# Optimization experiments

Measured on AMD Instinct MI355X. Metric: run time of the kernel, lower is better.

The kernel has to match this reference:

```python
import jax, jax.numpy as jnp
import numpy as np

H = 100  # hidden size

def _lstm_layer(x, Wih, Whh, b):
    # x: [B, T, D_in]; Wih: [4H, D_in]; Whh: [4H, H]; b: [4H]
    # Precompute input contribution for all timesteps (batched GEMM).
    xw = jnp.einsum('btd,gd->btg', x, Wih) + b            # [B, T, 4H]
    B = x.shape[0]
    h0 = jnp.zeros((B, H), x.dtype)
    c0 = jnp.zeros((B, H), x.dtype)
    WhhT = Whh.T                                          # [H, 4H]

    def step(carry, xw_t):
        h, c = carry
        gates = xw_t + h @ WhhT                           # [B, 4H]
        i, f, g, o = jnp.split(gates, 4, axis=-1)         # PyTorch order i,f,g,o
        i = jax.nn.sigmoid(i)
        f = jax.nn.sigmoid(f)
        g = jnp.tanh(g)
        o = jax.nn.sigmoid(o)
        c = f * c + i * g
        h = o * jnp.tanh(c)
        return (h, c), h

    _, hs = jax.lax.scan(step, (h0, c0), jnp.swapaxes(xw, 0, 1))  # [T, B, H]
    return jnp.swapaxes(hs, 0, 1)                         # [B, T, H]


def setup_inputs() -> dict:
    key = jax.random.key(0)
    ks = jax.random.split(key, 12)
    B, T = 512, 512
    s = 0.08  # small init scale to avoid gate saturation
    return {
        'z':    jax.random.normal(ks[0], (B, T, 1), jnp.float32),
        'Wih0': jax.random.normal(ks[1], (4 * H, 1), jnp.float32) * s,
        'Whh0': jax.random.normal(ks[2], (4 * H, H), jnp.float32) * s,
        'b0':   jax.random.normal(ks[3], (4 * H,), jnp.float32) * s,
        'Wih1': jax.random.normal(ks[4], (4 * H, H), jnp.float32) * s,
        'Whh1': jax.random.normal(ks[5], (4 * H, H), jnp.float32) * s,
        'b1':   jax.random.normal(ks[6], (4 * H,), jnp.float32) * s,
        'Wih2': jax.random.normal(ks[7], (4 * H, H), jnp.float32) * s,
        'Whh2': jax.random.normal(ks[8], (4 * H, H), jnp.float32) * s,
        'b2':   jax.random.normal(ks[9], (4 * H,), jnp.float32) * s,
        'Wp':   jax.random.normal(ks[10], (1, H), jnp.float32) * s,
        'bp':   jax.random.normal(ks[11], (1,), jnp.float32) * s,
    }


def reference(z, Wih0, Whh0, b0, Wih1, Whh1, b1, Wih2, Whh2, b2, Wp, bp):
    h = _lstm_layer(z, Wih0, Whh0, b0)
    h = _lstm_layer(h, Wih1, Whh1, b1)
    h = _lstm_layer(h, Wih2, Whh2, b2)       # [B, T, H]
    return jnp.tanh(jnp.einsum('bth,oh->bto', h, Wp) + bp)  # [B, T, 1]
```

## Files before the change

kernel.cpp:

```cpp
#include <hip/hip_runtime.h>
#include <cstdint>
#include <cstddef>


#define HH 100
#define G4 400
#define NB 512
#define NT 512
#define NBG 32
#define NTILE 25
#define KP 128

typedef _Float16 f16;
typedef _Float16 f16x8 __attribute__((ext_vector_type(8)));
typedef float f32x4 __attribute__((ext_vector_type(4)));

__device__ __forceinline__ float sigm(float x) { return 1.0f / (1.0f + __expf(-x)); }
__device__ __forceinline__ float tanh_(float x) { return 1.0f - 2.0f / (__expf(2.0f * x) + 1.0f); }

#define PIN22 __attribute__((amdgpu_flat_work_group_size(512, 512), \
                             amdgpu_waves_per_eu(2, 2)))

__device__ __forceinline__ int hswz(int b2, int u) {
  return b2 * KP + ((((u >> 3) ^ (b2 & 7)) << 3) | (u & 7));
}
__device__ __forceinline__ int bswz(int b2, int j) {
  return b2 * KP + ((j ^ (b2 & 7)) << 3);
}

__global__ __launch_bounds__(256) void wprep(
    const float* __restrict__ Whh0, const float* __restrict__ Whh1,
    const float* __restrict__ Whh2, const float* __restrict__ Wih1,
    const float* __restrict__ Wih2, const float* __restrict__ b1,
    const float* __restrict__ b2, const float* __restrict__ Wih0,
    const float* __restrict__ b0,
    f16* __restrict__ wfA, f16* __restrict__ wfI,
    float* __restrict__ biasf, float* __restrict__ l0w, float* __restrict__ l0b)
{
  int idx = blockIdx.x * 256 + threadIdx.x;
  if (idx < 153600) {
    int l = idx / 51200, r = idx % 51200;
    int nt = r / 2048, r2 = r % 2048;
    int kt = r2 / 512, r3 = r2 % 512;
    int lane = r3 / 8, j = r3 % 8;
    int mp = nt * 16 + (lane & 15);
    int grow = (mp & 3) * HH + (mp >> 2);
    int k = kt * 32 + (lane >> 4) * 8 + j;
    const float* W = (l == 0) ? Whh0 : ((l == 1) ? Whh1 : Whh2);
    wfA[idx] = (k < HH) ? (f16)W[grow * HH + k] : (f16)0.0f;
    return;
  }
  idx -= 153600;
  if (idx < 102400) {
    int l = idx / 51200, r = idx % 51200;
    int nt = r / 2048, r2 = r % 2048;
    int kt = r2 / 512, r3 = r2 % 512;
    int lane = r3 / 8, j = r3 % 8;
    int mp = nt * 16 + (lane & 15);
    int grow = (mp & 3) * HH + (mp >> 2);
    int k = kt * 32 + (lane >> 4) * 8 + j;
    const float* W = (l == 0) ? Wih1 : Wih2;
    wfI[idx] = (k < HH) ? (f16)W[grow * HH + k] : (f16)0.0f;
    return;
  }
  idx -= 102400;
  if (idx < 12800) {
    int l = idx / 6400, r = idx % 6400;
    int nt = r / 256, r2 = r % 256;
    int lane = r2 / 4, rr = r2 % 4;
    int mp = nt * 16 + (lane >> 4) * 4 + rr;
    int grow = (mp & 3) * HH + (mp >> 2);
    biasf[idx] = ((l == 0) ? b1 : b2)[grow];
    return;
  }
  idx -= 12800;
  if (idx < 12800) {
    int w = idx / 6400, r = idx % 6400;
    int nt = r / 256, r2 = r % 256;
    int lane = r2 / 4, rr = r2 % 4;
    int mp = nt * 16 + (lane >> 4) * 4 + rr;
    int grow = (mp & 3) * HH + (mp >> 2);
    if (w == 0) l0w[r] = Wih0[grow];
    else        l0b[r] = b0[grow];
  }
}

__global__ PIN22 void xwp(
    const float* __restrict__ hbufT,
    const f16* __restrict__ wfIl,
    const float* __restrict__ biasl,
    float* __restrict__ xwf,
    int t0, int CT)
{
  const int tid = threadIdx.x;
  const int w = tid >> 6, lane = tid & 63;
  const int nblk = CT / 8;
  const int bg = blockIdx.x / nblk, ts = blockIdx.x % nblk;
  const int tb = t0 + ts * 8;
  const int br = lane & 15, lg = lane >> 4;

  __shared__ __align__(16) f16 x16[8][16 * KP];

  {
    uint32_t* p = (uint32_t*)&x16[0][0];
    for (int i = tid; i < 8 * 16 * KP / 2; i += 512) p[i] = 0u;
  }
  __syncthreads();
  for (int i = tid; i < 8 * HH * 16; i += 512) {
    int t = i / 1600, r = i % 1600;
    int u = r >> 4, b2 = r & 15;
    float v = hbufT[(((size_t)bg * NT + (tb + t)) * HH + u) * 16 + b2];
    x16[t][hswz(b2, u)] = (f16)v;
  }

  const int NS = (w == 7) ? 4 : 3;
  const int tbase = 3 * w;

  f16x8 A[4][4];
  f32x4 bias4[4];
#pragma unroll
  for (int s = 0; s < 4; ++s) {
    if (s < NS) {
      int nt = tbase + s;
#pragma unroll
      for (int kt = 0; kt < 4; ++kt)
        A[s][kt] = *(const f16x8*)(wfIl + ((nt * 4 + kt) * 64 + lane) * 8);
      bias4[s] = *(const f32x4*)(biasl + (nt * 64 + lane) * 4);
    }
  }
  __syncthreads();

  for (int t = 0; t < 8; ++t) {
    f16x8 B[4];
#pragma unroll
    for (int kt = 0; kt < 4; ++kt)
      B[kt] = *(const f16x8*)(&x16[t][bswz(br, (kt << 2) + lg)]);
    const int tc = ts * 8 + t;
#pragma unroll
    for (int s = 0; s < 4; ++s) {
      if (s < NS) {
        f32x4 acc = bias4[s];
#pragma unroll
        for (int kt = 0; kt < 4; ++kt)
          acc = __builtin_amdgcn_mfma_f32_16x16x32_f16(A[s][kt], B[kt], acc, 0, 0, 0);
        int nt = tbase + s;
        *(f32x4*)(xwf + ((((size_t)bg * CT + tc) * NTILE + nt) * 64 + lane) * 4) = acc;
      }
    }
  }
}

__global__ PIN22 void recx(
    const float* __restrict__ xwf,
    const f16* __restrict__ wfAl,
    float* __restrict__ hbufT,
    float* __restrict__ cbuf,
    int t0, int CT)
{
  const int tid = threadIdx.x;
  const int w = tid >> 6, lane = tid & 63;
  const int bg = blockIdx.x;
  const int br = lane & 15, lg = lane >> 4;
  const int NS = (w == 0) ? 4 : 3;

  __shared__ __align__(16) f16 hHi[2][16 * KP];
  __shared__ __align__(16) f16 hLo[2][16 * KP];

  {
    uint32_t* p0 = (uint32_t*)&hHi[0][0];
    uint32_t* p1 = (uint32_t*)&hLo[0][0];
    for (int i = tid; i < 2 * 16 * KP / 2; i += 512) { p0[i] = 0u; p1[i] = 0u; }
  }
  __syncthreads();
  if (t0 > 0) {
    for (int i = tid; i < HH * 16; i += 512) {
      int u = i >> 4, b2 = i & 15;
      float v = hbufT[(((size_t)bg * NT + (t0 - 1)) * HH + u) * 16 + b2];
      f16 hi = (f16)v;
      hHi[0][hswz(b2, u)] = hi;
      hLo[0][hswz(b2, u)] = (f16)(v - (float)hi);
    }
  }

  f16x8 A[4][4];
  float c[4] = {0.f, 0.f, 0.f, 0.f};
  f32x4 xwC[4], xwN[4];
#pragma unroll
  for (int s = 0; s < 4; ++s) {
    if (s < NS) {
      const int nt = w + 8 * s;
#pragma unroll
      for (int kt = 0; kt < 4; ++kt)
        A[s][kt] = *(const f16x8*)(wfAl + ((nt * 4 + kt) * 64 + lane) * 8);
      if (t0 > 0) c[s] = cbuf[((size_t)bg * NTILE + nt) * 64 + lane];
      xwC[s] = *(const f32x4*)(xwf + (((size_t)bg * CT * NTILE + nt) * 64 + lane) * 4);
    }
  }
  __syncthreads();

  int cur = 0;
  for (int t = 0; t < CT; ++t) {
    f16x8 Bhi[4], Blo[4];
#pragma unroll
    for (int kt = 0; kt < 4; ++kt) {
      const int pos = bswz(br, (kt << 2) + lg);
      Bhi[kt] = *(const f16x8*)(&hHi[cur][pos]);
      Blo[kt] = *(const f16x8*)(&hLo[cur][pos]);
    }
    const int tn = (t + 1 < CT) ? t + 1 : t;
#pragma unroll
    for (int s = 0; s < 4; ++s) {
      if (s < NS) {
        const int nt = w + 8 * s;
        xwN[s] = *(const f32x4*)(xwf + ((((size_t)bg * CT + tn) * NTILE + nt) * 64 + lane) * 4);
      }
    }
#pragma unroll
    for (int s = 0; s < 4; ++s) {
      if (s < NS) {
        const int nt = w + 8 * s;
        f32x4 ah = xwC[s];
        f32x4 al = {0.f, 0.f, 0.f, 0.f};
#pragma unroll
        for (int kt = 0; kt < 4; ++kt) {
          ah = __builtin_amdgcn_mfma_f32_16x16x32_f16(A[s][kt], Bhi[kt], ah, 0, 0, 0);
          al = __builtin_amdgcn_mfma_f32_16x16x32_f16(A[s][kt], Blo[kt], al, 0, 0, 0);
        }
        f32x4 acc = ah + al;
        float iv = sigm(acc.x);
        float fv = sigm(acc.y);
        float gv = tanh_(acc.z);
        float ov = sigm(acc.w);
        c[s] = fv * c[s] + iv * gv;
        float hv = ov * tanh_(c[s]);
        const int u = nt * 4 + lg;
        hbufT[(((size_t)bg * NT + (t0 + t)) * HH + u) * 16 + br] = hv;
        f16 hi = (f16)hv;
        hHi[cur ^ 1][hswz(br, u)] = hi;
        hLo[cur ^ 1][hswz(br, u)] = (f16)(hv - (float)hi);
      }
    }
    __syncthreads();
#pragma unroll
    for (int s = 0; s < 4; ++s) xwC[s] = xwN[s];
    cur ^= 1;
  }
#pragma unroll
  for (int s = 0; s < 4; ++s) {
    if (s < NS) {
      const int nt = w + 8 * s;
      cbuf[((size_t)bg * NTILE + nt) * 64 + lane] = c[s];
    }
  }
}

__global__ PIN22 void rec0(
    const float* __restrict__ z,
    const float* __restrict__ l0w,
    const float* __restrict__ l0b,
    const f16* __restrict__ wfA0,
    float* __restrict__ hbufT)
{
  const int tid = threadIdx.x;
  const int w = tid >> 6, lane = tid & 63;
  const int bg = blockIdx.x;
  const int br = lane & 15, lg = lane >> 4;
  const int NS = (w == 0) ? 4 : 3;

  __shared__ __align__(16) f16 hHi[2][16 * KP];
  __shared__ __align__(16) f16 hLo[2][16 * KP];
  __shared__ __align__(16) float zl[NT][16];

  {
    uint32_t* p0 = (uint32_t*)&hHi[0][0];
    uint32_t* p1 = (uint32_t*)&hLo[0][0];
    for (int i = tid; i < 2 * 16 * KP / 2; i += 512) { p0[i] = 0u; p1[i] = 0u; }
  }
  for (int i = tid; i < 16 * NT; i += 512) {
    int j = i / NT, t = i % NT;
    zl[t][j] = z[(size_t)(bg * 16 + j) * NT + t];
  }

  f16x8 A[4][4];
  float c[4] = {0.f, 0.f, 0.f, 0.f};
  f32x4 wv[4], bv[4];
#pragma unroll
  for (int s = 0; s < 4; ++s) {
    if (s < NS) {
      const int nt = w + 8 * s;
#pragma unroll
      for (int kt = 0; kt < 4; ++kt)
        A[s][kt] = *(const f16x8*)(wfA0 + ((nt * 4 + kt) * 64 + lane) * 8);
      wv[s] = *(const f32x4*)(l0w + (nt * 64 + lane) * 4);
      bv[s] = *(const f32x4*)(l0b + (nt * 64 + lane) * 4);
    }
  }
  __syncthreads();

  int cur = 0;
  for (int t = 0; t < NT; ++t) {
    f16x8 Bhi[4], Blo[4];
#pragma unroll
    for (int kt = 0; kt < 4; ++kt) {
      const int pos = bswz(br, (kt << 2) + lg);
      Bhi[kt] = *(const f16x8*)(&hHi[cur][pos]);
      Blo[kt] = *(const f16x8*)(&hLo[cur][pos]);
    }
    const float zv = zl[t][br];
#pragma unroll
    for (int s = 0; s < 4; ++s) {
      if (s < NS) {
        const int nt = w + 8 * s;
        f32x4 ah = bv[s] + wv[s] * zv;
        f32x4 al = {0.f, 0.f, 0.f, 0.f};
#pragma unroll
        for (int kt = 0; kt < 4; ++kt) {
          ah = __builtin_amdgcn_mfma_f32_16x16x32_f16(A[s][kt], Bhi[kt], ah, 0, 0, 0);
          al = __builtin_amdgcn_mfma_f32_16x16x32_f16(A[s][kt], Blo[kt], al, 0, 0, 0);
        }
        f32x4 acc = ah + al;
        float iv = sigm(acc.x);
        float fv = sigm(acc.y);
        float gv = tanh_(acc.z);
        float ov = sigm(acc.w);
        c[s] = fv * c[s] + iv * gv;
        float hv = ov * tanh_(c[s]);
        const int u = nt * 4 + lg;
        hbufT[(((size_t)bg * NT + t) * HH + u) * 16 + br] = hv;
        f16 hi = (f16)hv;
        hHi[cur ^ 1][hswz(br, u)] = hi;
        hLo[cur ^ 1][hswz(br, u)] = (f16)(hv - (float)hi);
      }
    }
    __syncthreads();
    cur ^= 1;
  }
}

__global__ __launch_bounds__(256) void proj(
    const float* __restrict__ hbufT,
    const float* __restrict__ Wp, const float* __restrict__ bp,
    float* __restrict__ out)
{
  const int tid = threadIdx.x;
  const int bg = blockIdx.x >> 5, tsub = blockIdx.x & 31;
  const int br = tid & 15, tl = tid >> 4;
  const int t = tsub * 16 + tl;
  const float* hp = hbufT + (((size_t)bg * NT + t) * HH) * 16 + br;
  float acc = 0.0f;
#pragma unroll 4
  for (int u = 0; u < HH; ++u) acc += hp[u * 16] * Wp[u];
  out[(size_t)(bg * 16 + br) * NT + t] = tanh_(acc + bp[0]);
}

extern "C" void kernel_launch(void* const* d_in, const int* in_sizes, int n_in,
                              void* d_out, int out_size, void* d_ws, size_t ws_size,
                              hipStream_t stream) {
  const float* z    = (const float*)d_in[0];
  const float* Wih0 = (const float*)d_in[1];
  const float* Whh0 = (const float*)d_in[2];
  const float* b0   = (const float*)d_in[3];
  const float* Wih1 = (const float*)d_in[4];
  const float* Whh1 = (const float*)d_in[5];
  const float* b1   = (const float*)d_in[6];
  const float* Wih2 = (const float*)d_in[7];
  const float* Whh2 = (const float*)d_in[8];
  const float* b2   = (const float*)d_in[9];
  const float* Wp   = (const float*)d_in[10];
  const float* bp   = (const float*)d_in[11];
  float* out = (float*)d_out;

  float* ws = (float*)d_ws;
  float* hbufT = ws;
  float* cbuf  = ws + 26214400;
  f16*   wfA   = (f16*)(ws + 26265600);
  f16*   wfI   = (f16*)(ws + 26342400);
  float* biasf = ws + 26393600;
  float* l0w   = ws + 26406400;
  float* l0b   = ws + 26412800;
  float* xwf   = ws + 26419200;

  const size_t fixed = 26419200;
  int CT = 16;
  for (int c : {128, 64, 32, 16}) {
    if ((fixed + (size_t)NBG * c * 6400) * 4 <= ws_size) { CT = c; break; }
  }

  wprep<<<1100, 256, 0, stream>>>(Whh0, Whh1, Whh2, Wih1, Wih2, b1, b2,
                                  Wih0, b0, wfA, wfI, biasf, l0w, l0b);

  rec0<<<NBG, 512, 0, stream>>>(z, l0w, l0b, wfA, hbufT);

  for (int l = 0; l < 2; ++l) {
    const f16* wfAl = wfA + (size_t)(l + 1) * 51200;
    const f16* wfIl = wfI + (size_t)l * 51200;
    const float* bfl = biasf + (size_t)l * 6400;
    for (int t0 = 0; t0 < NT; t0 += CT) {
      xwp<<<NBG * (CT / 8), 512, 0, stream>>>(hbufT, wfIl, bfl, xwf, t0, CT);
      recx<<<NBG, 512, 0, stream>>>(xwf, wfAl, hbufT, cbuf, t0, CT);
    }
  }

  proj<<<1024, 256, 0, stream>>>(hbufT, Wp, bp, out);
}
```

Baseline: 3.042 ms.

## Fuse three LSTM layers into one persistent wavefront-pipelined kernel with ring buffers

The three LSTM layers now run inside a single persistent kernel of 96 blocks, one per layer and batch group. Each block hands its per-timestep hidden states to the next layer through a small f16 ring buffer in global memory, with producer and consumer counters updated by acquire/release atomics. This lets the layers run concurrently as a wavefront instead of serially. It also removes the many xwp/recx launches and the xw round-trip through memory, because the input projection is computed inline with MFMA. The costs are spin-wait synchronization between blocks, the requirement that all 96 blocks are co-resident (otherwise it deadlocks), and f16 rounding of the inter-layer inputs.

```diff
diff --git a/kernel.cpp b/kernel.cpp
--- a/kernel.cpp
+++ b/kernel.cpp
@@ -10,6 +10,8 @@
 #define NBG 32
 #define NTILE 25
 #define KP 128
+#define XROW 104
+#define RW 16
 
 typedef _Float16 f16;
 typedef _Float16 f16x8 __attribute__((ext_vector_type(8)));
@@ -21,11 +23,28 @@
 #define PIN22 __attribute__((amdgpu_flat_work_group_size(512, 512), \
                              amdgpu_waves_per_eu(2, 2)))
 
+__device__ __forceinline__ void spin_ge(const uint32_t* p, uint32_t v) {
+  while (__hip_atomic_load(p, __ATOMIC_ACQUIRE, __HIP_MEMORY_SCOPE_AGENT) < v)
+    __builtin_amdgcn_s_sleep(2);
+}
+__device__ __forceinline__ void rel_store(uint32_t* p, uint32_t v) {
+  __hip_atomic_store(p, v, __ATOMIC_RELEASE, __HIP_MEMORY_SCOPE_AGENT);
+}
+
 __device__ __forceinline__ int hswz(int b2, int u) {
   return b2 * KP + ((((u >> 3) ^ (b2 & 7)) << 3) | (u & 7));
 }
 __device__ __forceinline__ int bswz(int b2, int j) {
   return b2 * KP + ((j ^ (b2 & 7)) << 3);
+}
+
+__global__ __launch_bounds__(256) void initk(uint32_t* __restrict__ ring_u32,
+                                             uint32_t* __restrict__ cnts) {
+  const int n_ring = 2 * NBG * RW * 16 * XROW / 2;
+  for (int i = blockIdx.x * 256 + threadIdx.x; i < n_ring; i += gridDim.x * 256)
+    ring_u32[i] = 0u;
+  int i = blockIdx.x * 256 + threadIdx.x;
+  if (i < 2048) cnts[i] = 0u;
 }
 
 __global__ __launch_bounds__(256) void wprep(
@@ -46,8 +65,8 @@
     int mp = nt * 16 + (lane & 15);
     int grow = (mp & 3) * HH + (mp >> 2);
     int k = kt * 32 + (lane >> 4) * 8 + j;
-    const float* W = (l == 0) ? Whh0 : ((l == 1) ? Whh1 : Whh2);
-    wfA[idx] = (k < HH) ? (f16)W[grow * HH + k] : (f16)0.0f;
+    const float* Wm = (l == 0) ? Whh0 : ((l == 1) ? Whh1 : Whh2);
+    wfA[idx] = (k < HH) ? (f16)Wm[grow * HH + k] : (f16)0.0f;
     return;
   }
   idx -= 153600;
@@ -59,8 +78,8 @@
     int mp = nt * 16 + (lane & 15);
     int grow = (mp & 3) * HH + (mp >> 2);
     int k = kt * 32 + (lane >> 4) * 8 + j;
-    const float* W = (l == 0) ? Wih1 : Wih2;
-    wfI[idx] = (k < HH) ? (f16)W[grow * HH + k] : (f16)0.0f;
+    const float* Wm = (l == 0) ? Wih1 : Wih2;
+    wfI[idx] = (k < HH) ? (f16)Wm[grow * HH + k] : (f16)0.0f;
     return;
   }
   idx -= 102400;
@@ -85,106 +104,45 @@
   }
 }
 
-__global__ PIN22 void xwp(
-    const float* __restrict__ hbufT,
-    const f16* __restrict__ wfIl,
-    const float* __restrict__ biasl,
-    float* __restrict__ xwf,
-    int t0, int CT)
+__global__ PIN22 void lstm3(
+    const float* __restrict__ z,
+    const float* __restrict__ l0w,
+    const float* __restrict__ l0b,
+    const f16* __restrict__ wfA,
+    const f16* __restrict__ wfI,
+    const float* __restrict__ biasf,
+    f16* __restrict__ ring,
+    float* __restrict__ hbufT,
+    uint32_t* __restrict__ prodc,
+    uint32_t* __restrict__ consc)
 {
   const int tid = threadIdx.x;
   const int w = tid >> 6, lane = tid & 63;
-  const int nblk = CT / 8;
-  const int bg = blockIdx.x / nblk, ts = blockIdx.x % nblk;
-  const int tb = t0 + ts * 8;
-  const int br = lane & 15, lg = lane >> 4;
-
-  __shared__ __align__(16) f16 x16[8][16 * KP];
-
-  {
-    uint32_t* p = (uint32_t*)&x16[0][0];
-    for (int i = tid; i < 8 * 16 * KP / 2; i += 512) p[i] = 0u;
-  }
-  __syncthreads();
-  for (int i = tid; i < 8 * HH * 16; i += 512) {
-    int t = i / 1600, r = i % 1600;
-    int u = r >> 4, b2 = r & 15;
-    float v = hbufT[(((size_t)bg * NT + (tb + t)) * HH + u) * 16 + b2];
-    x16[t][hswz(b2, u)] = (f16)v;
-  }
-
-  const int NS = (w == 7) ? 4 : 3;
-  const int tbase = 3 * w;
-
-  f16x8 A[4][4];
-  f32x4 bias4[4];
-#pragma unroll
-  for (int s = 0; s < 4; ++s) {
-    if (s < NS) {
-      int nt = tbase + s;
-#pragma unroll
-      for (int kt = 0; kt < 4; ++kt)
-        A[s][kt] = *(const f16x8*)(wfIl + ((nt * 4 + kt) * 64 + lane) * 8);
-      bias4[s] = *(const f32x4*)(biasl + (nt * 64 + lane) * 4);
-    }
-  }
-  __syncthreads();
-
-  for (int t = 0; t < 8; ++t) {
-    f16x8 B[4];
-#pragma unroll
-    for (int kt = 0; kt < 4; ++kt)
-      B[kt] = *(const f16x8*)(&x16[t][bswz(br, (kt << 2) + lg)]);
-    const int tc = ts * 8 + t;
-#pragma unroll
-    for (int s = 0; s < 4; ++s) {
-      if (s < NS) {
-        f32x4 acc = bias4[s];
-#pragma unroll
-        for (int kt = 0; kt < 4; ++kt)
-          acc = __builtin_amdgcn_mfma_f32_16x16x32_f16(A[s][kt], B[kt], acc, 0, 0, 0);
-        int nt = tbase + s;
-        *(f32x4*)(xwf + ((((size_t)bg * CT + tc) * NTILE + nt) * 64 + lane) * 4) = acc;
-      }
-    }
-  }
-}
-
-__global__ PIN22 void recx(
-    const float* __restrict__ xwf,
-    const f16* __restrict__ wfAl,
-    float* __restrict__ hbufT,
-    float* __restrict__ cbuf,
-    int t0, int CT)
-{
-  const int tid = threadIdx.x;
-  const int w = tid >> 6, lane = tid & 63;
-  const int bg = blockIdx.x;
+  const int layer = blockIdx.x >> 5;
+  const int bg = blockIdx.x & 31;
   const int br = lane & 15, lg = lane >> 4;
   const int NS = (w == 0) ? 4 : 3;
 
   __shared__ __align__(16) f16 hHi[2][16 * KP];
   __shared__ __align__(16) f16 hLo[2][16 * KP];
+  __shared__ __align__(16) float zl[NT][16];
 
   {
     uint32_t* p0 = (uint32_t*)&hHi[0][0];
     uint32_t* p1 = (uint32_t*)&hLo[0][0];
     for (int i = tid; i < 2 * 16 * KP / 2; i += 512) { p0[i] = 0u; p1[i] = 0u; }
   }
-  __syncthreads();
-  if (t0 > 0) {
-    for (int i = tid; i < HH * 16; i += 512) {
-      int u = i >> 4, b2 = i & 15;
-      float v = hbufT[(((size_t)bg * NT + (t0 - 1)) * HH + u) * 16 + b2];
-      f16 hi = (f16)v;
-      hHi[0][hswz(b2, u)] = hi;
-      hLo[0][hswz(b2, u)] = (f16)(v - (float)hi);
-    }
-  }
-
-  f16x8 A[4][4];
+  if (layer == 0) {
+    for (int i = tid; i < 16 * NT; i += 512) {
+      int j = i / NT, t = i % NT;
+      zl[t][j] = z[(size_t)(bg * 16 + j) * NT + t];
+    }
+  }
+
+  const f16* wfAl = wfA + (size_t)layer * 51200;
+  f16x8 A[4][4], AI[4][4];
+  f32x4 wv[4], bv[4], bias4[4];
   float c[4] = {0.f, 0.f, 0.f, 0.f};
-  f32x4 xwC[4], xwN[4];
 #pragma unroll
   for (int s = 0; s < 4; ++s) {
     if (s < NS) {
@@ -192,14 +150,37 @@
 #pragma unroll
       for (int kt = 0; kt < 4; ++kt)
         A[s][kt] = *(const f16x8*)(wfAl + ((nt * 4 + kt) * 64 + lane) * 8);
-      if (t0 > 0) c[s] = cbuf[((size_t)bg * NTILE + nt) * 64 + lane];
-      xwC[s] = *(const f32x4*)(xwf + (((size_t)bg * CT * NTILE + nt) * 64 + lane) * 4);
-    }
+      if (layer == 0) {
+        wv[s] = *(const f32x4*)(l0w + (nt * 64 + lane) * 4);
+        bv[s] = *(const f32x4*)(l0b + (nt * 64 + lane) * 4);
+      } else {
+        const f16* wfIl = wfI + (size_t)(layer - 1) * 51200;
+#pragma unroll
+        for (int kt = 0; kt < 4; ++kt)
+          AI[s][kt] = *(const f16x8*)(wfIl + ((nt * 4 + kt) * 64 + lane) * 8);
+        bias4[s] = *(const f32x4*)(biasf + (size_t)(layer - 1) * 6400 + (nt * 64 + lane) * 4);
+      }
+    }
+  }
+
+  uint32_t* myProd = prodc + ((size_t)layer * NBG + bg) * 16;
+  uint32_t* myCons = consc + ((size_t)layer * NBG + bg) * 16;
+  const uint32_t* upProd = prodc + ((size_t)(layer - 1) * NBG + bg) * 16;
+  uint32_t* upCons = consc + ((size_t)(layer - 1) * NBG + bg) * 16;
+  f16* myPipe = ring + ((size_t)layer * NBG + bg) * RW * 16 * XROW;
+  const f16* srcPipe = ring + ((size_t)(layer - 1) * NBG + bg) * RW * 16 * XROW;
+
+  f16x8 Bx[4];
+  if (layer >= 1) {
+    spin_ge(upProd, 1u);
+#pragma unroll
+    for (int kt = 0; kt < 4; ++kt)
+      Bx[kt] = *(const f16x8*)(srcPipe + br * XROW + kt * 32 + lg * 8);
   }
   __syncthreads();
 
   int cur = 0;
-  for (int t = 0; t < CT; ++t) {
+  for (int t = 0; t < NT; ++t) {
     f16x8 Bhi[4], Blo[4];
 #pragma unroll
     for (int kt = 0; kt < 4; ++kt) {
@@ -207,19 +188,33 @@
       Bhi[kt] = *(const f16x8*)(&hHi[cur][pos]);
       Blo[kt] = *(const f16x8*)(&hLo[cur][pos]);
     }
-    const int tn = (t + 1 < CT) ? t + 1 : t;
+    f32x4 ax[4];
+    if (layer >= 1) {
+#pragma unroll
+      for (int s = 0; s < 4; ++s) {
+        if (s < NS) {
+          f32x4 a = {0.f, 0.f, 0.f, 0.f};
+#pragma unroll
+          for (int kt = 0; kt < 4; ++kt)
+            a = __builtin_amdgcn_mfma_f32_16x16x32_f16(AI[s][kt], Bx[kt], a, 0, 0, 0);
+          ax[s] = a;
+        }
+      }
+      if (t + 1 < NT) {
+        spin_ge(upProd, (uint32_t)(t + 2));
+        const f16* sb = srcPipe + (size_t)((t + 1) & (RW - 1)) * 16 * XROW;
+#pragma unroll
+        for (int kt = 0; kt < 4; ++kt)
+          Bx[kt] = *(const f16x8*)(sb + br * XROW + kt * 32 + lg * 8);
+      }
+    }
+    if (layer < 2 && t >= RW) spin_ge(myCons, (uint32_t)(t - RW + 1));
+
 #pragma unroll
     for (int s = 0; s < 4; ++s) {
       if (s < NS) {
         const int nt = w + 8 * s;
-        xwN[s] = *(const f32x4*)(xwf + ((((size_t)bg * CT + tn) * NTILE + nt) * 64 + lane) * 4);
-      }
-    }
-#pragma unroll
-    for (int s = 0; s < 4; ++s) {
-      if (s < NS) {
-        const int nt = w + 8 * s;
-        f32x4 ah = xwC[s];
+        f32x4 ah = (layer == 0) ? (bv[s] + wv[s] * zl[t][br]) : bias4[s];
         f32x4 al = {0.f, 0.f, 0.f, 0.f};
 #pragma unroll
         for (int kt = 0; kt < 4; ++kt) {
@@ -227,6 +222,7 @@
           al = __builtin_amdgcn_mfma_f32_16x16x32_f16(A[s][kt], Blo[kt], al, 0, 0, 0);
         }
         f32x4 acc = ah + al;
+        if (layer >= 1) acc = acc + ax[s];
         float iv = sigm(acc.x);
         float fv = sigm(acc.y);
         float gv = tanh_(acc.z);
@@ -234,105 +230,21 @@
         c[s] = fv * c[s] + iv * gv;
         float hv = ov * tanh_(c[s]);
         const int u = nt * 4 + lg;
-        hbufT[(((size_t)bg * NT + (t0 + t)) * HH + u) * 16 + br] = hv;
+        if (layer < 2) {
+          myPipe[(size_t)(t & (RW - 1)) * 16 * XROW + br * XROW + u] = (f16)hv;
+        } else {
+          hbufT[(((size_t)bg * NT + t) * HH + u) * 16 + br] = hv;
+        }
         f16 hi = (f16)hv;
         hHi[cur ^ 1][hswz(br, u)] = hi;
         hLo[cur ^ 1][hswz(br, u)] = (f16)(hv - (float)hi);
       }
     }
     __syncthreads();
-#pragma unroll
-    for (int s = 0; s < 4; ++s) xwC[s] = xwN[s];
-    cur ^= 1;
-  }
-#pragma unroll
-  for (int s = 0; s < 4; ++s) {
-    if (s < NS) {
-      const int nt = w + 8 * s;
-      cbuf[((size_t)bg * NTILE + nt) * 64 + lane] = c[s];
-    }
-  }
-}
-
-__global__ PIN22 void rec0(
-    const float* __restrict__ z,
-    const float* __restrict__ l0w,
-    const float* __restrict__ l0b,
-    const f16* __restrict__ wfA0,
-    float* __restrict__ hbufT)
-{
-  const int tid = threadIdx.x;
-  const int w = tid >> 6, lane = tid & 63;
-  const int bg = blockIdx.x;
-  const int br = lane & 15, lg = lane >> 4;
-  const int NS = (w == 0) ? 4 : 3;
-
-  __shared__ __align__(16) f16 hHi[2][16 * KP];
-  __shared__ __align__(16) f16 hLo[2][16 * KP];
-  __shared__ __align__(16) float zl[NT][16];
-
-  {
-    uint32_t* p0 = (uint32_t*)&hHi[0][0];
-    uint32_t* p1 = (uint32_t*)&hLo[0][0];
-    for (int i = tid; i < 2 * 16 * KP / 2; i += 512) { p0[i] = 0u; p1[i] = 0u; }
-  }
-  for (int i = tid; i < 16 * NT; i += 512) {
-    int j = i / NT, t = i % NT;
-    zl[t][j] = z[(size_t)(bg * 16 + j) * NT + t];
-  }
-
-  f16x8 A[4][4];
-  float c[4] = {0.f, 0.f, 0.f, 0.f};
-  f32x4 wv[4], bv[4];
-#pragma unroll
-  for (int s = 0; s < 4; ++s) {
-    if (s < NS) {
-      const int nt = w + 8 * s;
-#pragma unroll
-      for (int kt = 0; kt < 4; ++kt)
-        A[s][kt] = *(const f16x8*)(wfA0 + ((nt * 4 + kt) * 64 + lane) * 8);
-      wv[s] = *(const f32x4*)(l0w + (nt * 64 + lane) * 4);
-      bv[s] = *(const f32x4*)(l0b + (nt * 64 + lane) * 4);
-    }
-  }
-  __syncthreads();
-
-  int cur = 0;
-  for (int t = 0; t < NT; ++t) {
-    f16x8 Bhi[4], Blo[4];
-#pragma unroll
-    for (int kt = 0; kt < 4; ++kt) {
-      const int pos = bswz(br, (kt << 2) + lg);
-      Bhi[kt] = *(const f16x8*)(&hHi[cur][pos]);
-      Blo[kt] = *(const f16x8*)(&hLo[cur][pos]);
-    }
-    const float zv = zl[t][br];
-#pragma unroll
-    for (int s = 0; s < 4; ++s) {
-      if (s < NS) {
-        const int nt = w + 8 * s;
-        f32x4 ah = bv[s] + wv[s] * zv;
-        f32x4 al = {0.f, 0.f, 0.f, 0.f};
-#pragma unroll
-        for (int kt = 0; kt < 4; ++kt) {
-          ah = __builtin_amdgcn_mfma_f32_16x16x32_f16(A[s][kt], Bhi[kt], ah, 0, 0, 0);
-          al = __builtin_amdgcn_mfma_f32_16x16x32_f16(A[s][kt], Blo[kt], al, 0, 0, 0);
-        }
-        f32x4 acc = ah + al;
-        float iv = sigm(acc.x);
-        float fv = sigm(acc.y);
-        float gv = tanh_(acc.z);
-        float ov = sigm(acc.w);
-        c[s] = fv * c[s] + iv * gv;
-        float hv = ov * tanh_(c[s]);
-        const int u = nt * 4 + lg;
-        hbufT[(((size_t)bg * NT + t) * HH + u) * 16 + br] = hv;
-        f16 hi = (f16)hv;
-        hHi[cur ^ 1][hswz(br, u)] = hi;
-        hLo[cur ^ 1][hswz(br, u)] = (f16)(hv - (float)hi);
-      }
-    }
-    __syncthreads();
+    if (tid == 0) {
+      if (layer < 2) rel_store(myProd, (uint32_t)(t + 1));
+      if (layer >= 1) rel_store(upCons, (uint32_t)(t + 1));
+    }
     cur ^= 1;
   }
 }
@@ -371,35 +283,20 @@
   float* out = (float*)d_out;
 
   float* ws = (float*)d_ws;
-  float* hbufT = ws;
-  float* cbuf  = ws + 26214400;
-  f16*   wfA   = (f16*)(ws + 26265600);
-  f16*   wfI   = (f16*)(ws + 26342400);
-  float* biasf = ws + 26393600;
-  float* l0w   = ws + 26406400;
-  float* l0b   = ws + 26412800;
-  float* xwf   = ws + 26419200;
-
-  const size_t fixed = 26419200;
-  int CT = 16;
-  for (int c : {128, 64, 32, 16}) {
-    if ((fixed + (size_t)NBG * c * 6400) * 4 <= ws_size) { CT = c; break; }
-  }
-
+  float*    hbufT = ws;
+  f16*      ring  = (f16*)(ws + 26214400);
+  uint32_t* prodc = (uint32_t*)(ws + 26214400 + 851968);
+  uint32_t* consc = prodc + 1024;
+  f16*      wfA   = (f16*)(ws + 26214400 + 851968 + 2048);
+  f16*      wfI   = wfA + 153600;
+  float*    biasf = (float*)(wfI + 102400);
+  float*    l0w   = biasf + 12800;
+  float*    l0b   = l0w + 6400;
+
+  initk<<<2048, 256, 0, stream>>>((uint32_t*)ring, prodc);
   wprep<<<1100, 256, 0, stream>>>(Whh0, Whh1, Whh2, Wih1, Wih2, b1, b2,
                                   Wih0, b0, wfA, wfI, biasf, l0w, l0b);
-
-  rec0<<<NBG, 512, 0, stream>>>(z, l0w, l0b, wfA, hbufT);
-
-  for (int l = 0; l < 2; ++l) {
-    const f16* wfAl = wfA + (size_t)(l + 1) * 51200;
-    const f16* wfIl = wfI + (size_t)l * 51200;
-    const float* bfl = biasf + (size_t)l * 6400;
-    for (int t0 = 0; t0 < NT; t0 += CT) {
-      xwp<<<NBG * (CT / 8), 512, 0, stream>>>(hbufT, wfIl, bfl, xwf, t0, CT);
-      recx<<<NBG, 512, 0, stream>>>(xwf, wfAl, hbufT, cbuf, t0, CT);
-    }
-  }
-
+  lstm3<<<96, 512, 0, stream>>>(z, l0w, l0b, wfA, wfI, biasf,
+                                ring, hbufT, prodc, consc);
   proj<<<1024, 256, 0, stream>>>(hbufT, Wp, bp, out);
 }
```

New measurement: 7.913 ms. 2.6x slower.
